# Kernel optimization log

Hardware: AMD Instinct MI355X
Metric: run time of the kernel (lower is better)

## Reference

```python
import jax, jax.numpy as jnp
import numpy as np
from jax import lax

E, O, I, K = 8, 256, 128, 3  # num_experts, out_ch, in_ch, kernel
HID = 32  # routing hidden dim


def setup_inputs() -> dict:
    key = jax.random.key(0)
    ks = jax.random.split(key, 7)
    B, H, W = 32, 56, 56
    x = jax.random.normal(ks[0], (B, I, H, W), dtype=jnp.float32)
    # kaiming_normal fan_out for (E,O,I,K,K): fan_out = O*K*K
    std = float(np.sqrt(2.0 / (O * K * K)))
    weight = jax.random.normal(ks[1], (E, O, I, K, K), dtype=jnp.float32) * std
    bias = jax.random.normal(ks[2], (E, O), dtype=jnp.float32)
    # routing MLP: Linear(I,32) -> ReLU -> Linear(32,E) -> softmax
    w1 = jax.random.normal(ks[3], (HID, I), dtype=jnp.float32) / np.sqrt(I)
    b1 = jax.random.normal(ks[4], (HID,), dtype=jnp.float32) * 0.01
    w2 = jax.random.normal(ks[5], (E, HID), dtype=jnp.float32) / np.sqrt(HID)
    b2 = jax.random.normal(ks[6], (E,), dtype=jnp.float32) * 0.01
    return {"x": x, "weight": weight, "bias": bias, "w1": w1, "b1": b1, "w2": w2, "b2": b2}


def reference(x, weight, bias, w1, b1, w2, b2):
    # routing: global avg pool -> MLP -> softmax over experts
    pooled = x.mean(axis=(2, 3))                      # (B, I)
    h = jax.nn.relu(pooled @ w1.T + b1)               # (B, 32)
    r = jax.nn.softmax(h @ w2.T + b2, axis=1)         # (B, E)
    # per-sample combined kernel and bias
    cw = jnp.einsum('be,eoihw->boihw', r, weight)     # (B, O, I, K, K)
    cb = r @ bias                                     # (B, O)
    # per-sample conv (equivalent to groups=batch trick), stride=1, padding=1
    def conv_one(xi, wi):
        return lax.conv_general_dilated(
            xi[None], wi, window_strides=(1, 1), padding=[(1, 1), (1, 1)],
            dimension_numbers=('NCHW', 'OIHW', 'NCHW'))[0]
    out = jax.vmap(conv_one)(x, cw)                   # (B, O, H, W)
    return out + cb[:, :, None, None]
```

## Files before the change

### kernel.cpp

```cpp
#include <hip/hip_runtime.h>

#define E_ 8
#define O_ 256
#define I_ 128
#define B_ 32
#define H_ 56
#define W_ 56
#define HP 58
#define HW (H_*W_)
#define KK 9

#define NROW 4
#define NPIX 224
#define PPIX 348

typedef __attribute__((ext_vector_type(8))) short short8;
typedef __attribute__((ext_vector_type(4))) float float4_;

#define XP_ELEMS (B_*HP*HP*I_)
#define POOL_OFF ((size_t)XP_ELEMS*2)
#define R_OFF    (POOL_OFF + (size_t)B_*H_*I_*4)
#define CWT_OFF  (R_OFF + (size_t)B_*E_*4)

__device__ __forceinline__ unsigned short f2bf(float f) {
  union { float f; unsigned u; } v; v.f = f;
  unsigned r = v.u + 0x7FFFu + ((v.u >> 16) & 1u);
  return (unsigned short)(r >> 16);
}

__device__ __forceinline__ void gload16(const unsigned short* g, unsigned short* l) {
  __builtin_amdgcn_global_load_lds(
      (const __attribute__((address_space(1))) unsigned int*)g,
      (__attribute__((address_space(3))) unsigned int*)l, 16, 0, 0);
}

__global__ void k1_pool_pack(const float* __restrict__ x,
                             unsigned short* __restrict__ xp,
                             float* __restrict__ pooled_part) {
  __shared__ float lds[I_*57];
  const int h = blockIdx.x, b = blockIdx.y, tid = threadIdx.x;
  const float* xb = x + (size_t)b*I_*HW + h*W_;
  for (int idx = tid; idx < I_*W_; idx += 256) {
    int ic = idx / W_, wv = idx - ic*W_;
    lds[ic*57 + wv] = xb[(size_t)ic*HW + wv];
  }
  __syncthreads();
  if (tid < I_) {
    float s = 0.f;
    #pragma unroll 8
    for (int wv = 0; wv < W_; ++wv) s += lds[tid*57 + wv];
    pooled_part[(size_t)(b*H_ + h)*I_ + tid] = s;
  }
  unsigned short* xrow = xp + ((size_t)(b*HP + h + 1)*HP)*I_;
  for (int idx2 = tid; idx2 < W_*(I_/2); idx2 += 256) {
    int wv = idx2 >> 6, ic2 = idx2 & 63;
    unsigned short u0 = f2bf(lds[(ic2*2)*57 + wv]);
    unsigned short u1 = f2bf(lds[(ic2*2+1)*57 + wv]);
    *(unsigned*)&xrow[(wv+1)*I_ + ic2*2] = (unsigned)u0 | ((unsigned)u1 << 16);
  }
  if (tid < I_) {
    xrow[0*I_ + tid] = 0;
    xrow[57*I_ + tid] = 0;
  }
  if (h == 0) {
    unsigned short* r0 = xp + (size_t)(b*HP)*HP*I_;
    for (int idx = tid; idx < HP*I_; idx += 256) r0[idx] = 0;
  }
  if (h == H_-1) {
    unsigned short* r57 = xp + (size_t)((b*HP + 57)*HP)*I_;
    for (int idx = tid; idx < HP*I_; idx += 256) r57[idx] = 0;
  }
}

__global__ void k2_route(const float* __restrict__ pooled_part,
                         const float* __restrict__ w1, const float* __restrict__ b1,
                         const float* __restrict__ w2, const float* __restrict__ b2,
                         float* __restrict__ r) {
  __shared__ float p[I_];
  __shared__ float hh[32];
  __shared__ float lg[8];
  const int b = blockIdx.x, tid = threadIdx.x;
  if (tid < I_) {
    float s = 0.f;
    for (int h = 0; h < H_; ++h) s += pooled_part[(size_t)(b*H_ + h)*I_ + tid];
    p[tid] = s * (1.f/HW);
  }
  __syncthreads();
  if (tid < 32) {
    float s = b1[tid];
    for (int i = 0; i < I_; ++i) s += p[i]*w1[tid*I_ + i];
    hh[tid] = s > 0.f ? s : 0.f;
  }
  __syncthreads();
  if (tid < 8) {
    float s = b2[tid];
    for (int j = 0; j < 32; ++j) s += hh[j]*w2[tid*32 + j];
    lg[tid] = s;
  }
  __syncthreads();
  if (tid == 0) {
    float m = lg[0];
    for (int e = 1; e < 8; ++e) m = fmaxf(m, lg[e]);
    float ex[8], sum = 0.f;
    for (int e = 0; e < 8; ++e) { ex[e] = expf(lg[e]-m); sum += ex[e]; }
    float inv = 1.f/sum;
    for (int e = 0; e < 8; ++e) r[b*8 + e] = ex[e]*inv;
  }
}

__global__ void k3_combine(const float* __restrict__ weight, const float* __restrict__ r,
                           unsigned short* __restrict__ cwT) {
  __shared__ float wl[E_*1152];
  const int o = blockIdx.x, tid = threadIdx.x;
  const int b0 = blockIdx.y * 16;
  for (int e = 0; e < E_; ++e)
    for (int idx = tid; idx < 1152; idx += 256)
      wl[e*1152 + idx] = weight[(size_t)(e*O_ + o)*1152 + idx];
  __syncthreads();
  for (int b = b0; b < b0 + 16; ++b) {
    float rb[E_];
    #pragma unroll
    for (int e = 0; e < E_; ++e) rb[e] = r[b*E_ + e];
    for (int idx2 = tid; idx2 < 576; idx2 += 256) {
      int t = idx2 >> 6, ic2 = idx2 & 63;
      int ic = ic2*2;
      float v0 = 0.f, v1 = 0.f;
      #pragma unroll
      for (int e = 0; e < E_; ++e) {
        v0 += rb[e]*wl[e*1152 + ic*9 + t];
        v1 += rb[e]*wl[e*1152 + (ic+1)*9 + t];
      }
      *(unsigned*)&cwT[((size_t)(b*KK + t)*O_ + o)*I_ + ic] =
          (unsigned)f2bf(v0) | ((unsigned)f2bf(v1) << 16);
    }
  }
}

__global__ __launch_bounds__(256, 2)
void k4_conv(const unsigned short* __restrict__ xp,
             const unsigned short* __restrict__ cwT,
             const float* __restrict__ r, const float* __restrict__ bias,
             float* __restrict__ out) {
  __shared__ __align__(16) unsigned short patch[PPIX*64];
  __shared__ __align__(16) unsigned short ldsA[2][128*64];
  __shared__ float cbs[128];

  const int tid  = threadIdx.x;
  const int lane = tid & 63;
  const int wave = tid >> 6;
  const int gr0 = blockIdx.x * NROW;
  const int m0  = blockIdx.y * 128;
  const int b   = blockIdx.z;

  if (tid < 128) {
    float s = 0.f;
    #pragma unroll
    for (int e = 0; e < 8; ++e) s += r[b*8 + e]*bias[e*O_ + m0 + tid];
    cbs[tid] = s;
  }

  const int q = lane >> 4, l16 = lane & 15;
  const int lrow = lane >> 3, chunk = (lane & 7) ^ lrow;
  const int wm0 = (wave >> 1) * 64;
  const int wn0 = (wave & 1) * 112;

  int ainv[4];
  #pragma unroll
  for (int j = 0; j < 4; ++j)
    ainv[j] = (wave*32 + j*8 + lrow)*I_ + chunk*8;
  int rowA[4];
  #pragma unroll
  for (int f = 0; f < 4; ++f) rowA[f] = (wm0 + f*16 + l16)*64;
  int xq[2];
  #pragma unroll
  for (int s = 0; s < 2; ++s) xq[s] = ((s*4 + q) ^ (l16 & 7))*8;
  int bg[7];
  #pragma unroll
  for (int g = 0; g < 7; ++g) {
    int p = wn0 + g*16 + l16;
    int rr_ = p / 56;
    bg[g] = rr_*58 + (p - rr_*56);
  }

  float4_ acc[4][7];
  #pragma unroll
  for (int f = 0; f < 4; ++f)
    #pragma unroll
    for (int g = 0; g < 7; ++g) acc[f][g] = (float4_){0.f, 0.f, 0.f, 0.f};

  const unsigned short* xpb = xp + (size_t)((b*HP + gr0)*HP)*I_;

  for (int icc = 0; icc < 2; ++icc) {
    __syncthreads();
    for (int it = 0; it < 11; ++it) {
      int c = it*256 + tid;
      if (c < PPIX*8) {
        int pp = c >> 3, k8 = c & 7;
        short8 v = *(const short8*)(xpb + (size_t)pp*I_ + icc*64 + k8*8);
        *(short8*)&patch[pp*64 + ((k8 ^ (pp & 7))*8)] = v;
      }
    }
    {
      const unsigned short* ab = cwT + ((size_t)(b*KK)*O_ + m0)*I_ + icc*64;
      #pragma unroll
      for (int j = 0; j < 4; ++j)
        gload16(ab + ainv[j], &ldsA[0][(wave*32 + j*8)*64]);
    }
    for (int tap = 0; tap < 9; ++tap) {
      __syncthreads();
      if (tap < 8) {
        const unsigned short* ab = cwT + ((size_t)(b*KK + tap + 1)*O_ + m0)*I_ + icc*64;
        #pragma unroll
        for (int j = 0; j < 4; ++j)
          gload16(ab + ainv[j], &ldsA[(tap + 1) & 1][(wave*32 + j*8)*64]);
      }
      const unsigned short* At = ldsA[tap & 1];
      const int kh = tap / 3, kw = tap - kh*3;
      const int toff = kh*58 + kw;
      #pragma unroll
      for (int s = 0; s < 2; ++s) {
        short8 af[4], bfr[7];
        #pragma unroll
        for (int f = 0; f < 4; ++f) af[f] = *(const short8*)&At[rowA[f] + xq[s]];
        #pragma unroll
        for (int g = 0; g < 7; ++g) {
          int pp = bg[g] + toff;
          bfr[g] = *(const short8*)&patch[pp*64 + (((s*4 + q) ^ (pp & 7))*8)];
        }
        #pragma unroll
        for (int f = 0; f < 4; ++f)
          #pragma unroll
          for (int g = 0; g < 7; ++g)
            acc[f][g] = __builtin_amdgcn_mfma_f32_16x16x32_bf16(af[f], bfr[g], acc[f][g], 0, 0, 0);
      }
    }
  }

  const size_t obase = (size_t)(b*O_ + m0)*HW + gr0*W_;
  #pragma unroll
  for (int g = 0; g < 7; ++g) {
    int p = wn0 + g*16 + l16;
    #pragma unroll
    for (int f = 0; f < 4; ++f) {
      #pragma unroll
      for (int v = 0; v < 4; ++v) {
        int ml = wm0 + f*16 + q*4 + v;
        out[obase + (size_t)ml*HW + p] = acc[f][g][v] + cbs[ml];
      }
    }
  }
}

extern "C" void kernel_launch(void* const* d_in, const int* in_sizes, int n_in,
                              void* d_out, int out_size, void* d_ws, size_t ws_size,
                              hipStream_t stream) {
  const float* x      = (const float*)d_in[0];
  const float* weight = (const float*)d_in[1];
  const float* bias   = (const float*)d_in[2];
  const float* w1     = (const float*)d_in[3];
  const float* b1     = (const float*)d_in[4];
  const float* w2     = (const float*)d_in[5];
  const float* b2     = (const float*)d_in[6];
  float* out = (float*)d_out;
  char* ws = (char*)d_ws;

  unsigned short* xp     = (unsigned short*)(ws);
  float*          ppart  = (float*)(ws + POOL_OFF);
  float*          rr     = (float*)(ws + R_OFF);
  unsigned short* cwT    = (unsigned short*)(ws + CWT_OFF);

  k1_pool_pack<<<dim3(H_, B_), 256, 0, stream>>>(x, xp, ppart);
  k2_route<<<B_, 128, 0, stream>>>(ppart, w1, b1, w2, b2, rr);
  k3_combine<<<dim3(O_, 2), 256, 0, stream>>>(weight, rr, cwT);
  k4_conv<<<dim3(H_/NROW, 2, B_), 256, 0, stream>>>(xp, cwT, rr, bias, out);
}
```

Baseline: 258.4 us.

## Load conv weight fragments directly from global into registers, dropping LDS staging

Removes the double-buffered LDS staging of the combined weight tiles (global_load_lds plus a barrier per tap). Each lane now reads its A-fragments straight from global memory into registers and prefetches the next tap's first half one iteration ahead. This drops the per-tap __syncthreads and frees 32KB of LDS. In exchange there are more redundant global/L2 reads, since waves sharing rows each fetch their own copies, and the loads are exposed with less latency hiding.

```diff
diff --git a/kernel.cpp b/kernel.cpp
--- a/kernel.cpp
+++ b/kernel.cpp
@@ -26,12 +26,6 @@
   union { float f; unsigned u; } v; v.f = f;
   unsigned r = v.u + 0x7FFFu + ((v.u >> 16) & 1u);
   return (unsigned short)(r >> 16);
-}
-
-__device__ __forceinline__ void gload16(const unsigned short* g, unsigned short* l) {
-  __builtin_amdgcn_global_load_lds(
-      (const __attribute__((address_space(1))) unsigned int*)g,
-      (__attribute__((address_space(3))) unsigned int*)l, 16, 0, 0);
 }
 
 __global__ void k1_pool_pack(const float* __restrict__ x,
@@ -142,7 +136,6 @@
              const float* __restrict__ r, const float* __restrict__ bias,
              float* __restrict__ out) {
   __shared__ __align__(16) unsigned short patch[PPIX*64];
-  __shared__ __align__(16) unsigned short ldsA[2][128*64];
   __shared__ float cbs[128];
 
   const int tid  = threadIdx.x;
@@ -160,20 +153,13 @@
   }
 
   const int q = lane >> 4, l16 = lane & 15;
-  const int lrow = lane >> 3, chunk = (lane & 7) ^ lrow;
   const int wm0 = (wave >> 1) * 64;
   const int wn0 = (wave & 1) * 112;
 
-  int ainv[4];
-  #pragma unroll
-  for (int j = 0; j < 4; ++j)
-    ainv[j] = (wave*32 + j*8 + lrow)*I_ + chunk*8;
-  int rowA[4];
-  #pragma unroll
-  for (int f = 0; f < 4; ++f) rowA[f] = (wm0 + f*16 + l16)*64;
-  int xq[2];
-  #pragma unroll
-  for (int s = 0; s < 2; ++s) xq[s] = ((s*4 + q) ^ (l16 & 7))*8;
+  int arow[4];
+  #pragma unroll
+  for (int f = 0; f < 4; ++f)
+    arow[f] = (m0 + wm0 + f*16 + l16)*I_ + q*8;
   int bg[7];
   #pragma unroll
   for (int g = 0; g < 7; ++g) {
@@ -189,9 +175,14 @@
     for (int g = 0; g < 7; ++g) acc[f][g] = (float4_){0.f, 0.f, 0.f, 0.f};
 
   const unsigned short* xpb = xp + (size_t)((b*HP + gr0)*HP)*I_;
+  const unsigned short* cwb = cwT + (size_t)b*KK*O_*I_;
+
+  short8 afN[4];
+  #pragma unroll
+  for (int f = 0; f < 4; ++f) afN[f] = *(const short8*)(cwb + arow[f]);
 
   for (int icc = 0; icc < 2; ++icc) {
-    __syncthreads();
+    if (icc) __syncthreads();
     for (int it = 0; it < 11; ++it) {
       int c = it*256 + tid;
       if (c < PPIX*8) {
@@ -200,39 +191,44 @@
         *(short8*)&patch[pp*64 + ((k8 ^ (pp & 7))*8)] = v;
       }
     }
-    {
-      const unsigned short* ab = cwT + ((size_t)(b*KK)*O_ + m0)*I_ + icc*64;
-      #pragma unroll
-      for (int j = 0; j < 4; ++j)
-        gload16(ab + ainv[j], &ldsA[0][(wave*32 + j*8)*64]);
-    }
+    __syncthreads();
+
     for (int tap = 0; tap < 9; ++tap) {
-      __syncthreads();
+      const unsigned short* at = cwb + (size_t)tap*O_*I_ + icc*64;
+      short8 af0[4], af1[4];
+      #pragma unroll
+      for (int f = 0; f < 4; ++f) af0[f] = afN[f];
+      #pragma unroll
+      for (int f = 0; f < 4; ++f) af1[f] = *(const short8*)(at + arow[f] + 32);
       if (tap < 8) {
-        const unsigned short* ab = cwT + ((size_t)(b*KK + tap + 1)*O_ + m0)*I_ + icc*64;
-        #pragma unroll
-        for (int j = 0; j < 4; ++j)
-          gload16(ab + ainv[j], &ldsA[(tap + 1) & 1][(wave*32 + j*8)*64]);
-      }
-      const unsigned short* At = ldsA[tap & 1];
-      const int kh = tap / 3, kw = tap - kh*3;
-      const int toff = kh*58 + kw;
-      #pragma unroll
-      for (int s = 0; s < 2; ++s) {
-        short8 af[4], bfr[7];
-        #pragma unroll
-        for (int f = 0; f < 4; ++f) af[f] = *(const short8*)&At[rowA[f] + xq[s]];
-        #pragma unroll
-        for (int g = 0; g < 7; ++g) {
-          int pp = bg[g] + toff;
-          bfr[g] = *(const short8*)&patch[pp*64 + (((s*4 + q) ^ (pp & 7))*8)];
-        }
-        #pragma unroll
-        for (int f = 0; f < 4; ++f)
-          #pragma unroll
-          for (int g = 0; g < 7; ++g)
-            acc[f][g] = __builtin_amdgcn_mfma_f32_16x16x32_bf16(af[f], bfr[g], acc[f][g], 0, 0, 0);
-      }
+        #pragma unroll
+        for (int f = 0; f < 4; ++f) afN[f] = *(const short8*)(at + O_*I_ + arow[f]);
+      } else if (icc == 0) {
+        #pragma unroll
+        for (int f = 0; f < 4; ++f) afN[f] = *(const short8*)(cwb + 64 + arow[f]);
+      }
+      const int toff = (tap/3)*58 + (tap - (tap/3)*3);
+      short8 bfr[7];
+      #pragma unroll
+      for (int g = 0; g < 7; ++g) {
+        int pp = bg[g] + toff;
+        bfr[g] = *(const short8*)&patch[pp*64 + ((q ^ (pp & 7))*8)];
+      }
+      #pragma unroll
+      for (int f = 0; f < 4; ++f)
+        #pragma unroll
+        for (int g = 0; g < 7; ++g)
+          acc[f][g] = __builtin_amdgcn_mfma_f32_16x16x32_bf16(af0[f], bfr[g], acc[f][g], 0, 0, 0);
+      #pragma unroll
+      for (int g = 0; g < 7; ++g) {
+        int pp = bg[g] + toff;
+        bfr[g] = *(const short8*)&patch[pp*64 + (((4 + q) ^ (pp & 7))*8)];
+      }
+      #pragma unroll
+      for (int f = 0; f < 4; ++f)
+        #pragma unroll
+        for (int g = 0; g < 7; ++g)
+          acc[f][g] = __builtin_amdgcn_mfma_f32_16x16x32_bf16(af1[f], bfr[g], acc[f][g], 0, 0, 0);
     }
   }
 
```

Result: slower. 306.5 us (+18.6%).
